# Optimization experiments

Measured on AMD Instinct MI355X. Metric: run time of the kernel, lower is better.

## Reference

```python
import jax, jax.numpy as jnp
import numpy as np

L, D, H, FF = 4, 256, 8, 4 * 256  # num_layers, d_model, nhead, ffn hidden
DK = D // H
EPS = 1e-5


def _ln(x, g, b):
    mu = jnp.mean(x, axis=-1, keepdims=True)
    var = jnp.mean(jnp.square(x - mu), axis=-1, keepdims=True)
    return (x - mu) * jax.lax.rsqrt(var + EPS) * g + b


def setup_inputs() -> dict:
    key = jax.random.key(0)
    ks = jax.random.split(key, 16)
    B, N = 8, 1024
    s = 0.02
    return {
        "x": jax.random.normal(ks[0], (B, N, D), jnp.float32),
        "coords": jax.random.normal(ks[1], (B, N, 3), jnp.float32),
        "Wq": jax.random.normal(ks[2], (L, D, D), jnp.float32) * s,
        "bq": jnp.zeros((L, D), jnp.float32),
        "Wk": jax.random.normal(ks[3], (L, D, D), jnp.float32) * s,
        "bk": jnp.zeros((L, D), jnp.float32),
        "Wv": jax.random.normal(ks[4], (L, D, D), jnp.float32) * s,
        "bv": jnp.zeros((L, D), jnp.float32),
        "alpha": jnp.full((L,), 0.1, jnp.float32),
        "W1": jax.random.normal(ks[5], (L, D, FF), jnp.float32) * s,
        "b1": jnp.zeros((L, FF), jnp.float32),
        "W2": jax.random.normal(ks[6], (L, FF, D), jnp.float32) * s,
        "b2": jnp.zeros((L, D), jnp.float32),
        "g1": jnp.ones((L, D), jnp.float32),
        "be1": jnp.zeros((L, D), jnp.float32),
        "g2": jnp.ones((L, D), jnp.float32),
        "be2": jnp.zeros((L, D), jnp.float32),
    }


def reference(x, coords, Wq, bq, Wk, bk, Wv, bv, alpha, W1, b1, W2, b2, g1, be1, g2, be2):
    B, N, _ = x.shape
    # Per-batch pairwise coord dot products (same math as the BN x BN matmul
    # sliced per batch in the original, computed without the cross-batch waste).
    G0 = jnp.einsum("bnc,bmc->bnm", coords, coords)  # [B,N,N]
    scale = 1.0 / jnp.sqrt(jnp.float32(DK))
    for i in range(L):
        q = (x @ Wq[i] + bq[i]).reshape(B, N, H, DK)
        k = (x @ Wk[i] + bk[i]).reshape(B, N, H, DK)
        v = (x @ Wv[i] + bv[i]).reshape(B, N, H, DK)
        scores = jnp.einsum("bnhd,bmhd->bhnm", q, k) * scale + (alpha[i] * G0)[:, None]
        attn = jax.nn.softmax(scores, axis=-1)
        out = jnp.einsum("bhnm,bmhd->bnhd", attn, v).reshape(B, N, D)
        x = _ln(x + out, g1[i], be1[i])
        ff = jnp.maximum(x @ W1[i] + b1[i], 0.0) @ W2[i] + b2[i]
        x = _ln(x + ff, g2[i], be2[i])
    return x
```

## Files before the change

### kernel.cpp

```cpp
#include <hip/hip_runtime.h>
#include <hip/hip_bf16.h>

#define BB 8
#define NN 1024
#define DD 256
#define HH 8
#define DK 32
#define FFN 1024
#define NLAYERS 4
#define MM (BB * NN)
#define ROW_ELEMS (MM * DD)

#define QSCALE 0.2550655192922103f
#define LOG2E  1.4426950408889634f

typedef unsigned short ushort_t;
typedef __attribute__((ext_vector_type(8))) short bf16x8;
typedef __attribute__((ext_vector_type(4))) short bf16x4;
typedef __attribute__((ext_vector_type(4))) float f32x4;

__device__ __forceinline__ f32x4 mfma16(bf16x4 a, bf16x4 b, f32x4 c) {
#if __has_builtin(__builtin_amdgcn_mfma_f32_16x16x16bf16_1k)
    return __builtin_amdgcn_mfma_f32_16x16x16bf16_1k(a, b, c, 0, 0, 0);
#elif defined(__AMDGCN__)
    f32x4 d;
    asm volatile("v_mfma_f32_16x16x16_bf16 %0, %1, %2, %3"
                 : "=v"(d)
                 : "v"(a), "v"(b), "v"(c));
    return d;
#else
    return c;
#endif
}

__device__ __forceinline__ ushort_t f2b(float f) {
    __hip_bfloat16 h = __float2bfloat16(f);
    return *reinterpret_cast<ushort_t*>(&h);
}

__device__ __forceinline__ float fast_exp2(float x) {
#if __has_builtin(__builtin_amdgcn_exp2f)
    return __builtin_amdgcn_exp2f(x);
#else
    return exp2f(x);
#endif
}

__device__ __forceinline__ void async_ld16(const void* g, void* l) {
    __builtin_amdgcn_global_load_lds((const __attribute__((address_space(1))) void*)g,
                                     (__attribute__((address_space(3))) void*)l, 16, 0, 0);
}

#define PREP_BLOCKS (NLAYERS * 707)
#define COPY_BLOCKS (ROW_ELEMS / 4 / 256)
__global__ __launch_bounds__(256) void setup_kernel(const float* __restrict__ Wq,
                                                    const float* __restrict__ Wk,
                                                    const float* __restrict__ Wv,
                                                    const float* __restrict__ W1,
                                                    const float* __restrict__ W2,
                                                    const float* __restrict__ bq,
                                                    const float* __restrict__ bk,
                                                    const float* __restrict__ bv,
                                                    ushort_t* __restrict__ wqkvt,
                                                    ushort_t* __restrict__ w1t,
                                                    ushort_t* __restrict__ w2t,
                                                    float* __restrict__ bqkv,
                                                    const float4* __restrict__ in,
                                                    float4* __restrict__ xf,
                                                    ushort4* __restrict__ xb,
                                                    const float* __restrict__ coords,
                                                    ushort_t* __restrict__ Qa,
                                                    ushort_t* __restrict__ Ka) {
    const int tid = threadIdx.x;
    __shared__ float tile[32][33];

    if (blockIdx.x < PREP_BLOCKS) {
        const int id = blockIdx.x;
        const int layer = id / 707;
        const int r = id % 707;

        if (r >= 704) {
            const int chunk = r - 704;
            const float* src = (chunk == 0) ? bq : (chunk == 1) ? bk : bv;
            bqkv[layer * 768 + chunk * 256 + tid] = src[layer * 256 + tid];
            return;
        }

        const float* src;
        ushort_t* dst;
        int R, C, x, y;
        if (r < 192) {
            const int w = r >> 6, rr = r & 63;
            src = ((w == 0) ? Wq : (w == 1) ? Wk : Wv) + (size_t)layer * 65536;
            dst = wqkvt + (size_t)layer * 196608 + w * 65536;
            R = 256; C = 256; x = rr & 7; y = rr >> 3;
        } else if (r < 448) {
            const int rr = r - 192;
            src = W1 + (size_t)layer * 262144;
            dst = w1t + (size_t)layer * 262144;
            R = 256; C = 1024; x = rr & 31; y = rr >> 5;
        } else {
            const int rr = r - 448;
            src = W2 + (size_t)layer * 262144;
            dst = w2t + (size_t)layer * 262144;
            R = 1024; C = 256; x = rr & 7; y = rr >> 3;
        }
        const int r0 = y * 32, c0 = x * 32;
        const int tx = tid & 31, ty = tid >> 5;
#pragma unroll
        for (int i = 0; i < 4; ++i)
            tile[ty + 8 * i][tx] = src[(size_t)(r0 + ty + 8 * i) * C + (c0 + tx)];
        __syncthreads();
#pragma unroll
        for (int i = 0; i < 4; ++i)
            dst[(size_t)(c0 + ty + 8 * i) * R + (r0 + tx)] = f2b(tile[tx][ty + 8 * i]);
    } else {
        const int cb = blockIdx.x - PREP_BLOCKS;
        const int i = cb * 256 + tid;
        {
            float4 v = in[i];
            xf[i] = v;
            ushort4 b = {f2b(v.x), f2b(v.y), f2b(v.z), f2b(v.w)};
            xb[i] = b;
        }
        if (cb < 256) {
            const int id = cb * 256 + tid;
            const int bh = id >> 10, n = id & 1023;
            const int b = bh >> 3;
            ushort_t buf[32];
#pragma unroll
            for (int d = 0; d < 32; ++d) buf[d] = 0;
            buf[0] = f2b(coords[(size_t)(b * NN + n) * 3 + 0]);
            buf[1] = f2b(coords[(size_t)(b * NN + n) * 3 + 1]);
            buf[2] = f2b(coords[(size_t)(b * NN + n) * 3 + 2]);
            ushort_t* kp = Ka + ((size_t)bh * NN + n) * 64 + 32;
            ushort_t* qp = Qa + ((size_t)bh * NN + n) * 64 + 32;
            const uint4* b4 = (const uint4*)buf;
            uint4 z4 = {0u, 0u, 0u, 0u};
#pragma unroll
            for (int c = 0; c < 4; ++c) {
                *(uint4*)(kp + c * 8) = b4[c];
                *(uint4*)(qp + c * 8) = z4;
            }
        }
    }
}

template <int MODE, int BM>
__global__ __launch_bounds__(256) void mfma_gemm_kernel(const ushort_t* __restrict__ A,
                                                        const ushort_t* __restrict__ Bt,
                                                        const float* __restrict__ bias,
                                                        void* __restrict__ C0,
                                                        void* __restrict__ C1,
                                                        void* __restrict__ C2,
                                                        const float* __restrict__ coords,
                                                        const float* __restrict__ alpha, int layer,
                                                        int K, int ldc) {
    constexpr int NI = BM / 32;
    __shared__ ushort_t As0[2][BM * 32];
    __shared__ ushort_t As1[2][BM * 32];
    __shared__ ushort_t Bs0[2][128 * 32];
    __shared__ ushort_t Bs1[2][128 * 32];

    const int t    = threadIdx.x;
    const int bm   = blockIdx.y * BM;
    const int bn   = blockIdx.x * 128;
    const int wave = t >> 6, lane = t & 63;
    const int wm   = (wave >> 1) * (BM / 2), wn = (wave & 1) * 64;
    const int quad = lane >> 4, l16 = lane & 15;

    const int srow = t >> 2;
    const int scol = (t & 3) * 8;

    f32x4 acc[NI][4];
#pragma unroll
    for (int i = 0; i < NI; ++i)
#pragma unroll
        for (int j = 0; j < 4; ++j) {
            f32x4 z = {0.f, 0.f, 0.f, 0.f};
            acc[i][j] = z;
        }

    auto stage = [&](int pb, int k0) {
        async_ld16(A + (size_t)(bm + srow) * K + k0 + scol, As0[pb] + wave * 512);
        if constexpr (BM == 128)
            async_ld16(A + (size_t)(bm + 64 + srow) * K + k0 + scol, As0[pb] + 2048 + wave * 512);
        async_ld16(Bt + (size_t)(bn + srow) * K + k0 + scol, Bs0[pb] + wave * 512);
        async_ld16(Bt + (size_t)(bn + 64 + srow) * K + k0 + scol, Bs0[pb] + 2048 + wave * 512);
        async_ld16(A + (size_t)(bm + srow) * K + k0 + 32 + scol, As1[pb] + wave * 512);
        if constexpr (BM == 128)
            async_ld16(A + (size_t)(bm + 64 + srow) * K + k0 + 32 + scol, As1[pb] + 2048 + wave * 512);
        async_ld16(Bt + (size_t)(bn + srow) * K + k0 + 32 + scol, Bs1[pb] + wave * 512);
        async_ld16(Bt + (size_t)(bn + 64 + srow) * K + k0 + 32 + scol, Bs1[pb] + 2048 + wave * 512);
    };

    stage(0, 0);
    int pb = 0;
    for (int k0 = 0; k0 < K; k0 += 64, pb ^= 1) {
        __syncthreads();

        if (k0 + 64 < K) stage(pb ^ 1, k0 + 64);

        bf16x8 af0[NI], af1[NI], bf0[4], bf1[4];
#pragma unroll
        for (int i = 0; i < NI; ++i) {
            af0[i] = *(const bf16x8*)(As0[pb] + (wm + i * 16 + l16) * 32 + quad * 8);
            af1[i] = *(const bf16x8*)(As1[pb] + (wm + i * 16 + l16) * 32 + quad * 8);
        }
#pragma unroll
        for (int j = 0; j < 4; ++j) {
            bf0[j] = *(const bf16x8*)(Bs0[pb] + (wn + j * 16 + l16) * 32 + quad * 8);
            bf1[j] = *(const bf16x8*)(Bs1[pb] + (wn + j * 16 + l16) * 32 + quad * 8);
        }
#pragma unroll
        for (int i = 0; i < NI; ++i)
#pragma unroll
            for (int j = 0; j < 4; ++j) {
                acc[i][j] = __builtin_amdgcn_mfma_f32_16x16x32_bf16(af0[i], bf0[j], acc[i][j], 0, 0, 0);
                acc[i][j] = __builtin_amdgcn_mfma_f32_16x16x32_bf16(af1[i], bf1[j], acc[i][j], 0, 0, 0);
            }
    }

    const float av = (MODE == 2) ? alpha[layer] : 0.f;

#pragma unroll
    for (int j = 0; j < 4; ++j) {
        const int col = bn + wn + j * 16 + l16;
        const float bsv = bias[col];
#pragma unroll
        for (int i = 0; i < NI; ++i) {
            const int row0 = bm + wm + i * 16 + quad * 4;
            if (MODE == 2) {
                const int bb2 = row0 >> 10, nn0 = row0 & 1023;
                const int which = col >> 8, rem = col & 255;
                const int h = rem >> 5, d = rem & 31;
                const size_t bh = (size_t)((bb2 << 3) + h);
                if (which == 2) {
                    ushort4 pk;
                    pk.x = f2b(acc[i][j][0] + bsv);
                    pk.y = f2b(acc[i][j][1] + bsv);
                    pk.z = f2b(acc[i][j][2] + bsv);
                    pk.w = f2b(acc[i][j][3] + bsv);
                    *(ushort4*)&((ushort_t*)C2)[(bh * DK + d) * NN + nn0] = pk;
                } else {
#pragma unroll
                    for (int r = 0; r < 4; ++r) {
                        const float v = acc[i][j][r] + bsv;
                        const int nn = nn0 + r;
                        if (which == 0) {
                            ((ushort_t*)C0)[(bh * NN + nn) * 64 + d] = f2b(v * QSCALE);
                            if (d < 3)
                                ((ushort_t*)C0)[(bh * NN + nn) * 64 + 32 + d] =
                                    f2b(av * LOG2E * coords[(size_t)(bb2 * NN + nn) * 3 + d]);
                        } else {
                            ((ushort_t*)C1)[(bh * NN + nn) * 64 + d] = f2b(v);
                        }
                    }
                }
            } else {
#pragma unroll
                for (int r = 0; r < 4; ++r) {
                    float v = acc[i][j][r] + bsv;
                    if (MODE == 0)
                        ((float*)C0)[(size_t)(row0 + r) * ldc + col] = v;
                    else
                        ((ushort_t*)C0)[(size_t)(row0 + r) * ldc + col] = f2b(fmaxf(v, 0.f));
                }
            }
        }
    }
}

template <int DO_QKV>
__global__ __launch_bounds__(512) void ffn_ln_kernel(const float* __restrict__ aout,
                                                     const float* __restrict__ xfin,
                                                     const ushort_t* __restrict__ W1t,
                                                     const ushort_t* __restrict__ W2t,
                                                     const float* __restrict__ g1,
                                                     const float* __restrict__ be1,
                                                     const float* __restrict__ b1,
                                                     const float* __restrict__ b2,
                                                     const float* __restrict__ g2,
                                                     const float* __restrict__ be2,
                                                     float* __restrict__ xout,
                                                     const ushort_t* __restrict__ Wqkvt,
                                                     const float* __restrict__ bqkv,
                                                     const float* __restrict__ coords,
                                                     const float* __restrict__ alpha, int qlayer,
                                                     ushort_t* __restrict__ Qa,
                                                     ushort_t* __restrict__ Ka,
                                                     ushort_t* __restrict__ Vt) {
    __shared__ ushort_t Ha[8][32][32];
    __shared__ ushort_t Asf[8][32][32];
    __shared__ ushort_t Bs0[2][256 * 32];
    __shared__ ushort_t Bs1[2][256 * 32];
    __shared__ float Ya[32][260];
    __shared__ float redS[8][32];
    __shared__ float redQ[8][32];

    const int t = threadIdx.x;
    const int bm = blockIdx.x * 32;
    const int wave = t >> 6, lane = t & 63;
    const int quad = lane >> 4, l16 = lane & 15;
    const int wn = wave * 32;
    const int scol = (t & 3) * 8;

    auto stageB1 = [&](int pb, int nc, int ks) {
        const int nbase = nc * 256;
        const int k0 = ks * 64;
#pragma unroll
        for (int c = 0; c < 2; ++c) {
            const int brow = nbase + c * 128 + (t >> 2);
            async_ld16(W1t + (size_t)brow * 256 + k0 + scol, Bs0[pb] + c * 4096 + wave * 512);
            async_ld16(W1t + (size_t)brow * 256 + k0 + 32 + scol, Bs1[pb] + c * 4096 + wave * 512);
        }
    };
    auto stageB2 = [&](int pb, int nc, int ks) {
        const int k0 = nc * 256 + ks * 64;
#pragma unroll
        for (int c = 0; c < 2; ++c) {
            const int brow = c * 128 + (t >> 2);
            async_ld16(W2t + (size_t)brow * 1024 + k0 + scol, Bs0[pb] + c * 4096 + wave * 512);
            async_ld16(W2t + (size_t)brow * 1024 + k0 + 32 + scol, Bs1[pb] + c * 4096 + wave * 512);
        }
    };
    auto stage = [&](int pb, int st) {
        const int group = st >> 2, ks = st & 3, nc = group >> 1;
        if (!(group & 1)) stageB1(pb, nc, ks);
        else stageB2(pb, nc, ks);
    };
    auto stageQKV = [&](int pb, int qst) {
        const int chunk = qst >> 2, ks = qst & 3;
#pragma unroll
        for (int c = 0; c < 2; ++c) {
            const int brow = chunk * 256 + c * 128 + (t >> 2);
            async_ld16(Wqkvt + (size_t)brow * 256 + ks * 64 + scol, Bs0[pb] + c * 4096 + wave * 512);
            async_ld16(Wqkvt + (size_t)brow * 256 + ks * 64 + 32 + scol, Bs1[pb] + c * 4096 + wave * 512);
        }
    };

    stage(0, 0);

#pragma unroll
    for (int rr = 0; rr < 4; ++rr) {
        const int row = wave * 4 + rr;
        const size_t base = (size_t)(bm + row) * DD + lane * 4;

        float4 xv = *(const float4*)(xfin + base);
        float4 dl = *(const float4*)(aout + base);
        float v0 = xv.x + dl.x, v1 = xv.y + dl.y, v2 = xv.z + dl.z, v3 = xv.w + dl.w;

        float s = v0 + v1 + v2 + v3;
#pragma unroll
        for (int off = 32; off; off >>= 1) s += __shfl_xor(s, off);
        const float mean = s * (1.0f / 256.0f);

        float d0 = v0 - mean, d1 = v1 - mean, d2 = v2 - mean, d3 = v3 - mean;
        float s2 = d0 * d0 + d1 * d1 + d2 * d2 + d3 * d3;
#pragma unroll
        for (int off = 32; off; off >>= 1) s2 += __shfl_xor(s2, off);
        const float rs = rsqrtf(s2 * (1.0f / 256.0f) + 1e-5f);

        float4 gv = *(const float4*)(g1 + lane * 4);
        float4 bv = *(const float4*)(be1 + lane * 4);
        float y0 = d0 * rs * gv.x + bv.x;
        float y1 = d1 * rs * gv.y + bv.y;
        float y2 = d2 * rs * gv.z + bv.z;
        float y3 = d3 * rs * gv.w + bv.w;

        float4 yv = {y0, y1, y2, y3};
        *(float4*)&Ya[row][lane * 4] = yv;
        const int col0 = lane * 4;
        ushort4 yb = {f2b(y0), f2b(y1), f2b(y2), f2b(y3)};
        *(ushort4*)&Asf[col0 >> 5][row][col0 & 31] = yb;
    }

    f32x4 acc1[2][2], acc2[2][2];
#pragma unroll
    for (int i = 0; i < 2; ++i)
#pragma unroll
        for (int j = 0; j < 2; ++j) {
            f32x4 z = {0.f, 0.f, 0.f, 0.f};
            acc1[i][j] = z;
            acc2[i][j] = z;
        }

    int pb = 0;
    for (int st = 0; st < 32; ++st, pb ^= 1) {
        __syncthreads();
        if (st < 31) stage(pb ^ 1, st + 1);
        else if (DO_QKV) stageQKV(pb ^ 1, 0);

        const int group = st >> 2, ks = st & 3;
        const bool ff1 = !(group & 1);

        bf16x8 af0[2], af1[2], bf0[2], bf1[2];
#pragma unroll
        for (int i = 0; i < 2; ++i) {
            if (ff1) {
                af0[i] = *(const bf16x8*)&Asf[2 * ks][i * 16 + l16][quad * 8];
                af1[i] = *(const bf16x8*)&Asf[2 * ks + 1][i * 16 + l16][quad * 8];
            } else {
                af0[i] = *(const bf16x8*)&Ha[2 * ks][i * 16 + l16][quad * 8];
                af1[i] = *(const bf16x8*)&Ha[2 * ks + 1][i * 16 + l16][quad * 8];
            }
        }
#pragma unroll
        for (int j = 0; j < 2; ++j) {
            bf0[j] = *(const bf16x8*)(Bs0[pb] + (wn + j * 16 + l16) * 32 + quad * 8);
            bf1[j] = *(const bf16x8*)(Bs1[pb] + (wn + j * 16 + l16) * 32 + quad * 8);
        }

        if (ff1) {
#pragma unroll
            for (int i = 0; i < 2; ++i)
#pragma unroll
                for (int j = 0; j < 2; ++j) {
                    acc1[i][j] = __builtin_amdgcn_mfma_f32_16x16x32_bf16(af0[i], bf0[j], acc1[i][j], 0, 0, 0);
                    acc1[i][j] = __builtin_amdgcn_mfma_f32_16x16x32_bf16(af1[i], bf1[j], acc1[i][j], 0, 0, 0);
                }
            if (ks == 3) {
                const int nc = group >> 1;
#pragma unroll
                for (int j = 0; j < 2; ++j) {
                    const int col = nc * 256 + wn + j * 16 + l16;
                    const float bj = b1[col];
#pragma unroll
                    for (int i = 0; i < 2; ++i)
#pragma unroll
                        for (int r = 0; r < 4; ++r) {
                            const int row = i * 16 + quad * 4 + r;
                            Ha[wave][row][j * 16 + l16] =
                                f2b(fmaxf(acc1[i][j][r] + bj, 0.f));
                        }
                }
#pragma unroll
                for (int i = 0; i < 2; ++i)
#pragma unroll
                    for (int j = 0; j < 2; ++j) {
                        f32x4 z = {0.f, 0.f, 0.f, 0.f};
                        acc1[i][j] = z;
                    }
            }
        } else {
#pragma unroll
            for (int i = 0; i < 2; ++i)
#pragma unroll
                for (int j = 0; j < 2; ++j) {
                    acc2[i][j] = __builtin_amdgcn_mfma_f32_16x16x32_bf16(af0[i], bf0[j], acc2[i][j], 0, 0, 0);
                    acc2[i][j] = __builtin_amdgcn_mfma_f32_16x16x32_bf16(af1[i], bf1[j], acc2[i][j], 0, 0, 0);
                }
        }
    }

    float mean[2][4], rstd[2][4];

    {
        float sum_[2][4];
#pragma unroll
        for (int i = 0; i < 2; ++i)
#pragma unroll
            for (int r = 0; r < 4; ++r) sum_[i][r] = 0.f;
#pragma unroll
        for (int j = 0; j < 2; ++j) {
            const int col = wn + j * 16 + l16;
            const float bj = b2[col];
#pragma unroll
            for (int i = 0; i < 2; ++i) {
#pragma unroll
                for (int r = 0; r < 4; ++r) {
                    const int row = i * 16 + quad * 4 + r;
                    const float v = acc2[i][j][r] + bj + Ya[row][col];
                    acc2[i][j][r] = v;
                    sum_[i][r] += v;
                }
            }
        }
#pragma unroll
        for (int i = 0; i < 2; ++i)
#pragma unroll
            for (int r = 0; r < 4; ++r) {
                float s = sum_[i][r];
                s += __shfl_xor(s, 1);
                s += __shfl_xor(s, 2);
                s += __shfl_xor(s, 4);
                s += __shfl_xor(s, 8);
                sum_[i][r] = s;
            }
        if (l16 == 0) {
#pragma unroll
            for (int i = 0; i < 2; ++i)
#pragma unroll
                for (int r = 0; r < 4; ++r) redS[wave][i * 16 + quad * 4 + r] = sum_[i][r];
        }
        __syncthreads();
#pragma unroll
        for (int i = 0; i < 2; ++i)
#pragma unroll
            for (int r = 0; r < 4; ++r) {
                const int rl = i * 16 + quad * 4 + r;
                float s = 0.f;
#pragma unroll
                for (int w = 0; w < 8; ++w) s += redS[w][rl];
                mean[i][r] = s * (1.0f / 256.0f);
            }
    }

    {
        float sq_[2][4];
#pragma unroll
        for (int i = 0; i < 2; ++i)
#pragma unroll
            for (int r = 0; r < 4; ++r) sq_[i][r] = 0.f;
#pragma unroll
        for (int j = 0; j < 2; ++j)
#pragma unroll
            for (int i = 0; i < 2; ++i)
#pragma unroll
                for (int r = 0; r < 4; ++r) {
                    const float d = acc2[i][j][r] - mean[i][r];
                    sq_[i][r] += d * d;
                }
#pragma unroll
        for (int i = 0; i < 2; ++i)
#pragma unroll
            for (int r = 0; r < 4; ++r) {
                float s = sq_[i][r];
                s += __shfl_xor(s, 1);
                s += __shfl_xor(s, 2);
                s += __shfl_xor(s, 4);
                s += __shfl_xor(s, 8);
                sq_[i][r] = s;
            }
        if (l16 == 0) {
#pragma unroll
            for (int i = 0; i < 2; ++i)
#pragma unroll
                for (int r = 0; r < 4; ++r) redQ[wave][i * 16 + quad * 4 + r] = sq_[i][r];
        }
        __syncthreads();
#pragma unroll
        for (int i = 0; i < 2; ++i)
#pragma unroll
            for (int r = 0; r < 4; ++r) {
                const int rl = i * 16 + quad * 4 + r;
                float s = 0.f;
#pragma unroll
                for (int w = 0; w < 8; ++w) s += redQ[w][rl];
                rstd[i][r] = rsqrtf(s * (1.0f / 256.0f) + 1e-5f);
            }
    }

#pragma unroll
    for (int j = 0; j < 2; ++j) {
        const int col = wn + j * 16 + l16;
        const float gv = g2[col];
        const float bev = be2[col];
#pragma unroll
        for (int i = 0; i < 2; ++i) {
            const int row = bm + i * 16 + quad * 4;
#pragma unroll
            for (int r = 0; r < 4; ++r) {
                const float y = (acc2[i][j][r] - mean[i][r]) * rstd[i][r] * gv + bev;
                xout[(size_t)(row + r) * DD + col] = y;
                if (DO_QKV)
                    Asf[wave][i * 16 + quad * 4 + r][j * 16 + l16] = f2b(y);
            }
        }
    }

    if constexpr (DO_QKV) {
        const float av = alpha[qlayer];
        f32x4 acc3[2][2];
#pragma unroll
        for (int i = 0; i < 2; ++i)
#pragma unroll
            for (int j = 0; j < 2; ++j) {
                f32x4 z = {0.f, 0.f, 0.f, 0.f};
                acc3[i][j] = z;
            }

        for (int qst = 0; qst < 12; ++qst, pb ^= 1) {
            __syncthreads();
            if (qst < 11) stageQKV(pb ^ 1, qst + 1);

            const int ks = qst & 3;
            bf16x8 af0[2], af1[2], bf0[2], bf1[2];
#pragma unroll
            for (int i = 0; i < 2; ++i) {
                af0[i] = *(const bf16x8*)&Asf[2 * ks][i * 16 + l16][quad * 8];
                af1[i] = *(const bf16x8*)&Asf[2 * ks + 1][i * 16 + l16][quad * 8];
            }
#pragma unroll
            for (int j = 0; j < 2; ++j) {
                bf0[j] = *(const bf16x8*)(Bs0[pb] + (wn + j * 16 + l16) * 32 + quad * 8);
                bf1[j] = *(const bf16x8*)(Bs1[pb] + (wn + j * 16 + l16) * 32 + quad * 8);
            }
#pragma unroll
            for (int i = 0; i < 2; ++i)
#pragma unroll
                for (int j = 0; j < 2; ++j) {
                    acc3[i][j] = __builtin_amdgcn_mfma_f32_16x16x32_bf16(af0[i], bf0[j], acc3[i][j], 0, 0, 0);
                    acc3[i][j] = __builtin_amdgcn_mfma_f32_16x16x32_bf16(af1[i], bf1[j], acc3[i][j], 0, 0, 0);
                }

            if (ks == 3) {
                const int which = qst >> 2;
#pragma unroll
                for (int j = 0; j < 2; ++j) {
                    const int rem = wn + j * 16 + l16;
                    const float bsv = bqkv[which * 256 + rem];
                    const int h = rem >> 5, d = rem & 31;
#pragma unroll
                    for (int i = 0; i < 2; ++i) {
                        const int row0 = bm + i * 16 + quad * 4;
                        const int bb2 = row0 >> 10, nn0 = row0 & 1023;
                        const size_t bh = (size_t)((bb2 << 3) + h);
                        if (which == 2) {
                            ushort4 pk;
                            pk.x = f2b(acc3[i][j][0] + bsv);
                            pk.y = f2b(acc3[i][j][1] + bsv);
                            pk.z = f2b(acc3[i][j][2] + bsv);
                            pk.w = f2b(acc3[i][j][3] + bsv);
                            *(ushort4*)&Vt[(bh * DK + d) * NN + nn0] = pk;
                        } else {
#pragma unroll
                            for (int r = 0; r < 4; ++r) {
                                const float v = acc3[i][j][r] + bsv;
                                const int nn = nn0 + r;
                                if (which == 0) {
                                    Qa[(bh * NN + nn) * 64 + d] = f2b(v * QSCALE);
                                    if (d < 3)
                                        Qa[(bh * NN + nn) * 64 + 32 + d] =
                                            f2b(av * LOG2E *
                                                coords[(size_t)(bb2 * NN + nn) * 3 + d]);
                                } else {
                                    Ka[(bh * NN + nn) * 64 + d] = f2b(v);
                                }
                            }
                        }
                    }
                }
#pragma unroll
                for (int i = 0; i < 2; ++i)
#pragma unroll
                    for (int j = 0; j < 2; ++j) {
                        f32x4 z = {0.f, 0.f, 0.f, 0.f};
                        acc3[i][j] = z;
                    }
            }
        }
    }
}

__global__ __launch_bounds__(256, 2) void attn8_kernel(const ushort_t* __restrict__ Qa,
                                                       const ushort_t* __restrict__ Ka,
                                                       const ushort_t* __restrict__ Vt,
                                                       float* __restrict__ aout) {
    const int b = blockIdx.x, h = blockIdx.y, n0 = blockIdx.z * 64;
    const int t = threadIdx.x, wave = t >> 6, lane = t & 63;
    const int quad = lane >> 4, l16 = lane & 15;
    const int bh = b * HH + h;

    __shared__ __align__(16) char smem[56320];
    ushort_t (*Ks)[64][72] = (ushort_t (*)[64][72])smem;
    ushort_t (*Vs)[32][72] = (ushort_t (*)[32][72])(smem + 36864);
    float    (*Om)[64][36] = (float (*)[64][36])smem;
    float    (*Lm)[64]     = (float (*)[64])(smem + 55296);

    bf16x8 aq[4][2];
#pragma unroll
    for (int s = 0; s < 4; ++s) {
        const ushort_t* qp = Qa + ((size_t)bh * NN + n0 + s * 16 + l16) * 64 + quad * 8;
        aq[s][0] = *(const bf16x8*)qp;
        aq[s][1] = *(const bf16x8*)(qp + 32);
    }

    const f32x4 z = {0.f, 0.f, 0.f, 0.f};
    f32x4 acc[4][2];
    float lsum[4];
#pragma unroll
    for (int s = 0; s < 4; ++s) { acc[s][0] = z; acc[s][1] = z; lsum[s] = 0.f; }

    const ushort_t* kg = Ka + ((size_t)bh * NN + wave * 256) * 64;
    const ushort_t* vg = Vt + (size_t)bh * DK * NN + wave * 256;

    const int srow = lane >> 3, sch = (lane & 7) * 8;

    uint4 kreg[8], vreg[4];
#pragma unroll
    for (int i = 0; i < 8; ++i) kreg[i] = *(const uint4*)(kg + (size_t)(i * 8 + srow) * 64 + sch);
#pragma unroll
    for (int i = 0; i < 4; ++i) vreg[i] = *(const uint4*)(vg + (size_t)(i * 8 + srow) * NN + sch);

    for (int kt = 0; kt < 4; ++kt) {
#pragma unroll
        for (int i = 0; i < 8; ++i) *(uint4*)&Ks[wave][i * 8 + srow][sch] = kreg[i];
#pragma unroll
        for (int i = 0; i < 4; ++i) *(uint4*)&Vs[wave][i * 8 + srow][sch] = vreg[i];

        bf16x8 bk0[4], bk1[4];
#pragma unroll
        for (int jt = 0; jt < 4; ++jt) {
            bk0[jt] = *(const bf16x8*)&Ks[wave][jt * 16 + l16][quad * 8];
            bk1[jt] = *(const bf16x8*)&Ks[wave][jt * 16 + l16][32 + quad * 8];
        }
        bf16x4 vfrag[2][4];
#pragma unroll
        for (int g = 0; g < 2; ++g)
#pragma unroll
            for (int jt = 0; jt < 4; ++jt)
                vfrag[g][jt] = *(const bf16x4*)&Vs[wave][g * 16 + l16][jt * 16 + quad * 4];

        if (kt < 3) {
            const ushort_t* kg2 = kg + (size_t)(kt + 1) * 64 * 64;
            const ushort_t* vg2 = vg + (kt + 1) * 64;
#pragma unroll
            for (int i = 0; i < 8; ++i)
                kreg[i] = *(const uint4*)(kg2 + (size_t)(i * 8 + srow) * 64 + sch);
#pragma unroll
            for (int i = 0; i < 4; ++i)
                vreg[i] = *(const uint4*)(vg2 + (size_t)(i * 8 + srow) * NN + sch);
        }

#pragma unroll
        for (int s = 0; s < 4; ++s) {
            f32x4 st[4];
            __builtin_amdgcn_s_setprio(1);
#pragma unroll
            for (int jt = 0; jt < 4; ++jt) {
                st[jt] = __builtin_amdgcn_mfma_f32_16x16x32_bf16(bk0[jt], aq[s][0], z, 0, 0, 0);
                st[jt] = __builtin_amdgcn_mfma_f32_16x16x32_bf16(bk1[jt], aq[s][1], st[jt], 0, 0, 0);
            }
            __builtin_amdgcn_s_setprio(0);
            bf16x4 pf[4];
            float ls = 0.f;
#pragma unroll
            for (int jt = 0; jt < 4; ++jt) {
                float e0 = fast_exp2(st[jt][0]);
                float e1 = fast_exp2(st[jt][1]);
                float e2 = fast_exp2(st[jt][2]);
                float e3 = fast_exp2(st[jt][3]);
                ls += (e0 + e1) + (e2 + e3);
                pf[jt][0] = (short)f2b(e0);
                pf[jt][1] = (short)f2b(e1);
                pf[jt][2] = (short)f2b(e2);
                pf[jt][3] = (short)f2b(e3);
            }
            lsum[s] += ls;
            __builtin_amdgcn_s_setprio(1);
#pragma unroll
            for (int jt = 0; jt < 4; ++jt) {
                acc[s][0] = mfma16(vfrag[0][jt], pf[jt], acc[s][0]);
                acc[s][1] = mfma16(vfrag[1][jt], pf[jt], acc[s][1]);
            }
            __builtin_amdgcn_s_setprio(0);
        }
    }

#pragma unroll
    for (int s = 0; s < 4; ++s) {
        lsum[s] += __shfl_xor(lsum[s], 16);
        lsum[s] += __shfl_xor(lsum[s], 32);
    }

    __syncthreads();
    if (quad == 0) {
#pragma unroll
        for (int s = 0; s < 4; ++s) Lm[wave][s * 16 + l16] = lsum[s];
    }

#pragma unroll
    for (int s = 0; s < 4; ++s) {
        const int q = s * 16 + l16;
#pragma unroll
        for (int g = 0; g < 2; ++g) {
            float4 v = {acc[s][g][0], acc[s][g][1], acc[s][g][2], acc[s][g][3]};
            *(float4*)&Om[wave][q][g * 16 + quad * 4] = v;
        }
    }
    __syncthreads();

    {
        const int q = t >> 2, dseg = (t & 3) * 8;
        const float inv = 1.0f / (Lm[0][q] + Lm[1][q] + Lm[2][q] + Lm[3][q]);
        float* op = aout + (size_t)(b * NN + n0 + q) * DD + h * DK + dseg;
        float4 s0 = {0.f, 0.f, 0.f, 0.f}, s1 = {0.f, 0.f, 0.f, 0.f};
#pragma unroll
        for (int w = 0; w < 4; ++w) {
            float4 a = *(const float4*)&Om[w][q][dseg];
            float4 c = *(const float4*)&Om[w][q][dseg + 4];
            s0.x += a.x; s0.y += a.y; s0.z += a.z; s0.w += a.w;
            s1.x += c.x; s1.y += c.y; s1.z += c.z; s1.w += c.w;
        }
        float4 o0 = {s0.x * inv, s0.y * inv, s0.z * inv, s0.w * inv};
        float4 o1 = {s1.x * inv, s1.y * inv, s1.z * inv, s1.w * inv};
        *(float4*)op = o0;
        *(float4*)(op + 4) = o1;
    }
}

extern "C" void kernel_launch(void* const* d_in, const int* in_sizes, int n_in,
                              void* d_out, int out_size, void* d_ws, size_t ws_size,
                              hipStream_t stream) {
    const float* x      = (const float*)d_in[0];
    const float* coords = (const float*)d_in[1];
    const float* Wq     = (const float*)d_in[2];
    const float* bq     = (const float*)d_in[3];
    const float* Wk     = (const float*)d_in[4];
    const float* bk     = (const float*)d_in[5];
    const float* Wv     = (const float*)d_in[6];
    const float* bv     = (const float*)d_in[7];
    const float* alpha  = (const float*)d_in[8];
    const float* W1     = (const float*)d_in[9];
    const float* b1     = (const float*)d_in[10];
    const float* W2     = (const float*)d_in[11];
    const float* b2     = (const float*)d_in[12];
    const float* g1     = (const float*)d_in[13];
    const float* be1    = (const float*)d_in[14];
    const float* g2     = (const float*)d_in[15];
    const float* be2    = (const float*)d_in[16];

    float* ws = (float*)d_ws;
    float*    xf    = ws;
    ushort_t* xb    = (ushort_t*)(ws + 2097152);
    ushort_t* Qa    = (ushort_t*)(ws + 3145728);
    ushort_t* Ka    = (ushort_t*)(ws + 5242880);
    ushort_t* Vt    = (ushort_t*)(ws + 7340032);
    float*    aout  = ws + 8388608;
    ushort_t* wqkvt = (ushort_t*)(ws + 10485760);
    ushort_t* w1t   = (ushort_t*)(ws + 10878976);
    ushort_t* w2t   = (ushort_t*)(ws + 11403264);
    float*    bqkv  = ws + 11927552;

    setup_kernel<<<PREP_BLOCKS + COPY_BLOCKS, 256, 0, stream>>>(
        Wq, Wk, Wv, W1, W2, bq, bk, bv, wqkvt, w1t, w2t, bqkv,
        (const float4*)x, (float4*)xf, (ushort4*)xb, coords, Qa, Ka);

    mfma_gemm_kernel<2, 64><<<dim3(6, 128), 256, 0, stream>>>(
        xb, wqkvt, bqkv, Qa, Ka, Vt, coords, alpha, 0, 256, 0);

    for (int i = 0; i < NLAYERS; ++i) {
        attn8_kernel<<<dim3(8, 8, 16), 256, 0, stream>>>(Qa, Ka, Vt, aout);

        if (i < NLAYERS - 1) {
            ffn_ln_kernel<1><<<MM / 32, 512, 0, stream>>>(
                aout, xf, w1t + (size_t)i * 262144, w2t + (size_t)i * 262144,
                g1 + i * 256, be1 + i * 256, b1 + i * 1024, b2 + i * 256,
                g2 + i * 256, be2 + i * 256, xf,
                wqkvt + (size_t)(i + 1) * 196608, bqkv + (i + 1) * 768,
                coords, alpha, i + 1, Qa, Ka, Vt);
        } else {
            ffn_ln_kernel<0><<<MM / 32, 512, 0, stream>>>(
                aout, xf, w1t + (size_t)i * 262144, w2t + (size_t)i * 262144,
                g1 + i * 256, be1 + i * 256, b1 + i * 1024, b2 + i * 256,
                g2 + i * 256, be2 + i * 256, (float*)d_out,
                nullptr, nullptr, nullptr, nullptr, 0, nullptr, nullptr, nullptr);
        }
    }
}
```

Baseline: 359.7 us.

## Halve FFN row tile to 16 and single-buffer weight staging for occupancy

```diff
diff --git a/kernel.cpp b/kernel.cpp
--- a/kernel.cpp
+++ b/kernel.cpp
@@ -272,78 +272,78 @@
 }
 
 template <int DO_QKV>
-__global__ __launch_bounds__(512) void ffn_ln_kernel(const float* __restrict__ aout,
-                                                     const float* __restrict__ xfin,
-                                                     const ushort_t* __restrict__ W1t,
-                                                     const ushort_t* __restrict__ W2t,
-                                                     const float* __restrict__ g1,
-                                                     const float* __restrict__ be1,
-                                                     const float* __restrict__ b1,
-                                                     const float* __restrict__ b2,
-                                                     const float* __restrict__ g2,
-                                                     const float* __restrict__ be2,
-                                                     float* __restrict__ xout,
-                                                     const ushort_t* __restrict__ Wqkvt,
-                                                     const float* __restrict__ bqkv,
-                                                     const float* __restrict__ coords,
-                                                     const float* __restrict__ alpha, int qlayer,
-                                                     ushort_t* __restrict__ Qa,
-                                                     ushort_t* __restrict__ Ka,
-                                                     ushort_t* __restrict__ Vt) {
-    __shared__ ushort_t Ha[8][32][32];
-    __shared__ ushort_t Asf[8][32][32];
-    __shared__ ushort_t Bs0[2][256 * 32];
-    __shared__ ushort_t Bs1[2][256 * 32];
-    __shared__ float Ya[32][260];
-    __shared__ float redS[8][32];
-    __shared__ float redQ[8][32];
+__global__ __launch_bounds__(512, 4) void ffn_ln_kernel(const float* __restrict__ aout,
+                                                        const float* __restrict__ xfin,
+                                                        const ushort_t* __restrict__ W1t,
+                                                        const ushort_t* __restrict__ W2t,
+                                                        const float* __restrict__ g1,
+                                                        const float* __restrict__ be1,
+                                                        const float* __restrict__ b1,
+                                                        const float* __restrict__ b2,
+                                                        const float* __restrict__ g2,
+                                                        const float* __restrict__ be2,
+                                                        float* __restrict__ xout,
+                                                        const ushort_t* __restrict__ Wqkvt,
+                                                        const float* __restrict__ bqkv,
+                                                        const float* __restrict__ coords,
+                                                        const float* __restrict__ alpha, int qlayer,
+                                                        ushort_t* __restrict__ Qa,
+                                                        ushort_t* __restrict__ Ka,
+                                                        ushort_t* __restrict__ Vt) {
+    __shared__ ushort_t Ha[8][16][32];
+    __shared__ ushort_t Asf[8][16][32];
+    __shared__ ushort_t Bs0[256 * 32];
+    __shared__ ushort_t Bs1[256 * 32];
+    __shared__ float Ya[16][260];
+    __shared__ float redS[8][16];
+    __shared__ float redQ[8][16];
 
     const int t = threadIdx.x;
-    const int bm = blockIdx.x * 32;
+    const int bm = blockIdx.x * 16;
     const int wave = t >> 6, lane = t & 63;
     const int quad = lane >> 4, l16 = lane & 15;
     const int wn = wave * 32;
     const int scol = (t & 3) * 8;
 
-    auto stageB1 = [&](int pb, int nc, int ks) {
+    auto stageB1 = [&](int nc, int ks) {
         const int nbase = nc * 256;
         const int k0 = ks * 64;
 #pragma unroll
         for (int c = 0; c < 2; ++c) {
             const int brow = nbase + c * 128 + (t >> 2);
-            async_ld16(W1t + (size_t)brow * 256 + k0 + scol, Bs0[pb] + c * 4096 + wave * 512);
-            async_ld16(W1t + (size_t)brow * 256 + k0 + 32 + scol, Bs1[pb] + c * 4096 + wave * 512);
+            async_ld16(W1t + (size_t)brow * 256 + k0 + scol, Bs0 + c * 4096 + wave * 512);
+            async_ld16(W1t + (size_t)brow * 256 + k0 + 32 + scol, Bs1 + c * 4096 + wave * 512);
         }
     };
-    auto stageB2 = [&](int pb, int nc, int ks) {
+    auto stageB2 = [&](int nc, int ks) {
         const int k0 = nc * 256 + ks * 64;
 #pragma unroll
         for (int c = 0; c < 2; ++c) {
             const int brow = c * 128 + (t >> 2);
-            async_ld16(W2t + (size_t)brow * 1024 + k0 + scol, Bs0[pb] + c * 4096 + wave * 512);
-            async_ld16(W2t + (size_t)brow * 1024 + k0 + 32 + scol, Bs1[pb] + c * 4096 + wave * 512);
+            async_ld16(W2t + (size_t)brow * 1024 + k0 + scol, Bs0 + c * 4096 + wave * 512);
+            async_ld16(W2t + (size_t)brow * 1024 + k0 + 32 + scol, Bs1 + c * 4096 + wave * 512);
         }
     };
-    auto stage = [&](int pb, int st) {
+    auto stageFFN = [&](int st) {
         const int group = st >> 2, ks = st & 3, nc = group >> 1;
-        if (!(group & 1)) stageB1(pb, nc, ks);
-        else stageB2(pb, nc, ks);
+        if (!(group & 1)) stageB1(nc, ks);
+        else stageB2(nc, ks);
     };
-    auto stageQKV = [&](int pb, int qst) {
+    auto stageQKV = [&](int qst) {
         const int chunk = qst >> 2, ks = qst & 3;
 #pragma unroll
         for (int c = 0; c < 2; ++c) {
             const int brow = chunk * 256 + c * 128 + (t >> 2);
-            async_ld16(Wqkvt + (size_t)brow * 256 + ks * 64 + scol, Bs0[pb] + c * 4096 + wave * 512);
-            async_ld16(Wqkvt + (size_t)brow * 256 + ks * 64 + 32 + scol, Bs1[pb] + c * 4096 + wave * 512);
+            async_ld16(Wqkvt + (size_t)brow * 256 + ks * 64 + scol, Bs0 + c * 4096 + wave * 512);
+            async_ld16(Wqkvt + (size_t)brow * 256 + ks * 64 + 32 + scol, Bs1 + c * 4096 + wave * 512);
         }
     };
 
-    stage(0, 0);
-
-#pragma unroll
-    for (int rr = 0; rr < 4; ++rr) {
-        const int row = wave * 4 + rr;
+    stageFFN(0);
+
+#pragma unroll
+    for (int rr = 0; rr < 2; ++rr) {
+        const int row = wave * 2 + rr;
         const size_t base = (size_t)(bm + row) * DD + lane * 4;
 
         float4 xv = *(const float4*)(xfin + base);
@@ -375,50 +375,40 @@
         *(ushort4*)&Asf[col0 >> 5][row][col0 & 31] = yb;
     }
 
-    f32x4 acc1[2][2], acc2[2][2];
-#pragma unroll
-    for (int i = 0; i < 2; ++i)
-#pragma unroll
-        for (int j = 0; j < 2; ++j) {
-            f32x4 z = {0.f, 0.f, 0.f, 0.f};
-            acc1[i][j] = z;
-            acc2[i][j] = z;
-        }
-
-    int pb = 0;
-    for (int st = 0; st < 32; ++st, pb ^= 1) {
+    f32x4 acc1[2], acc2[2];
+#pragma unroll
+    for (int j = 0; j < 2; ++j) {
+        f32x4 z = {0.f, 0.f, 0.f, 0.f};
+        acc1[j] = z;
+        acc2[j] = z;
+    }
+
+    for (int st = 0; st < 32; ++st) {
         __syncthreads();
-        if (st < 31) stage(pb ^ 1, st + 1);
-        else if (DO_QKV) stageQKV(pb ^ 1, 0);
 
         const int group = st >> 2, ks = st & 3;
         const bool ff1 = !(group & 1);
 
-        bf16x8 af0[2], af1[2], bf0[2], bf1[2];
-#pragma unroll
-        for (int i = 0; i < 2; ++i) {
-            if (ff1) {
-                af0[i] = *(const bf16x8*)&Asf[2 * ks][i * 16 + l16][quad * 8];
-                af1[i] = *(const bf16x8*)&Asf[2 * ks + 1][i * 16 + l16][quad * 8];
-            } else {
-                af0[i] = *(const bf16x8*)&Ha[2 * ks][i * 16 + l16][quad * 8];
-                af1[i] = *(const bf16x8*)&Ha[2 * ks + 1][i * 16 + l16][quad * 8];
-            }
+        bf16x8 af0, af1, bf0[2], bf1[2];
+        if (ff1) {
+            af0 = *(const bf16x8*)&Asf[2 * ks][l16][quad * 8];
+            af1 = *(const bf16x8*)&Asf[2 * ks + 1][l16][quad * 8];
+        } else {
+            af0 = *(const bf16x8*)&Ha[2 * ks][l16][quad * 8];
+            af1 = *(const bf16x8*)&Ha[2 * ks + 1][l16][quad * 8];
         }
 #pragma unroll
         for (int j = 0; j < 2; ++j) {
-            bf0[j] = *(const bf16x8*)(Bs0[pb] + (wn + j * 16 + l16) * 32 + quad * 8);
-            bf1[j] = *(const bf16x8*)(Bs1[pb] + (wn + j * 16 + l16) * 32 + quad * 8);
+            bf0[j] = *(const bf16x8*)(Bs0 + (wn + j * 16 + l16) * 32 + quad * 8);
+            bf1[j] = *(const bf16x8*)(Bs1 + (wn + j * 16 + l16) * 32 + quad * 8);
         }
 
         if (ff1) {
 #pragma unroll
-            for (int i = 0; i < 2; ++i)
-#pragma unroll
-                for (int j = 0; j < 2; ++j) {
-                    acc1[i][j] = __builtin_amdgcn_mfma_f32_16x16x32_bf16(af0[i], bf0[j], acc1[i][j], 0, 0, 0);
-                    acc1[i][j] = __builtin_amdgcn_mfma_f32_16x16x32_bf16(af1[i], bf1[j], acc1[i][j], 0, 0, 0);
-                }
+            for (int j = 0; j < 2; ++j) {
+                acc1[j] = __builtin_amdgcn_mfma_f32_16x16x32_bf16(af0, bf0[j], acc1[j], 0, 0, 0);
+                acc1[j] = __builtin_amdgcn_mfma_f32_16x16x32_bf16(af1, bf1[j], acc1[j], 0, 0, 0);
+            }
             if (ks == 3) {
                 const int nc = group >> 1;
 #pragma unroll
@@ -426,129 +416,105 @@
                     const int col = nc * 256 + wn + j * 16 + l16;
                     const float bj = b1[col];
 #pragma unroll
-                    for (int i = 0; i < 2; ++i)
-#pragma unroll
-                        for (int r = 0; r < 4; ++r) {
-                            const int row = i * 16 + quad * 4 + r;
-                            Ha[wave][row][j * 16 + l16] =
-                                f2b(fmaxf(acc1[i][j][r] + bj, 0.f));
-                        }
+                    for (int r = 0; r < 4; ++r) {
+                        const int row = quad * 4 + r;
+                        Ha[wave][row][j * 16 + l16] = f2b(fmaxf(acc1[j][r] + bj, 0.f));
+                    }
                 }
 #pragma unroll
-                for (int i = 0; i < 2; ++i)
-#pragma unroll
-                    for (int j = 0; j < 2; ++j) {
-                        f32x4 z = {0.f, 0.f, 0.f, 0.f};
-                        acc1[i][j] = z;
-                    }
+                for (int j = 0; j < 2; ++j) {
+                    f32x4 z = {0.f, 0.f, 0.f, 0.f};
+                    acc1[j] = z;
+                }
             }
         } else {
 #pragma unroll
-            for (int i = 0; i < 2; ++i)
-#pragma unroll
-                for (int j = 0; j < 2; ++j) {
-                    acc2[i][j] = __builtin_amdgcn_mfma_f32_16x16x32_bf16(af0[i], bf0[j], acc2[i][j], 0, 0, 0);
-                    acc2[i][j] = __builtin_amdgcn_mfma_f32_16x16x32_bf16(af1[i], bf1[j], acc2[i][j], 0, 0, 0);
-                }
-        }
-    }
-
-    float mean[2][4], rstd[2][4];
+            for (int j = 0; j < 2; ++j) {
+                acc2[j] = __builtin_amdgcn_mfma_f32_16x16x32_bf16(af0, bf0[j], acc2[j], 0, 0, 0);
+                acc2[j] = __builtin_amdgcn_mfma_f32_16x16x32_bf16(af1, bf1[j], acc2[j], 0, 0, 0);
+            }
+        }
+
+        __syncthreads();
+        if (st + 1 < 32) stageFFN(st + 1);
+        else if (DO_QKV) stageQKV(0);
+    }
+
+    float mean[4], rstd[4];
 
     {
-        float sum_[2][4];
-#pragma unroll
-        for (int i = 0; i < 2; ++i)
-#pragma unroll
-            for (int r = 0; r < 4; ++r) sum_[i][r] = 0.f;
+        float sum_[4];
+#pragma unroll
+        for (int r = 0; r < 4; ++r) sum_[r] = 0.f;
 #pragma unroll
         for (int j = 0; j < 2; ++j) {
             const int col = wn + j * 16 + l16;
             const float bj = b2[col];
 #pragma unroll
-            for (int i = 0; i < 2; ++i) {
-#pragma unroll
-                for (int r = 0; r < 4; ++r) {
-                    const int row = i * 16 + quad * 4 + r;
-                    const float v = acc2[i][j][r] + bj + Ya[row][col];
-                    acc2[i][j][r] = v;
-                    sum_[i][r] += v;
-                }
-            }
-        }
-#pragma unroll
-        for (int i = 0; i < 2; ++i)
-#pragma unroll
             for (int r = 0; r < 4; ++r) {
-                float s = sum_[i][r];
-                s += __shfl_xor(s, 1);
-                s += __shfl_xor(s, 2);
-                s += __shfl_xor(s, 4);
-                s += __shfl_xor(s, 8);
-                sum_[i][r] = s;
-            }
+                const int row = quad * 4 + r;
+                const float v = acc2[j][r] + bj + Ya[row][col];
+                acc2[j][r] = v;
+                sum_[r] += v;
+            }
+        }
+#pragma unroll
+        for (int r = 0; r < 4; ++r) {
+            float s = sum_[r];
+            s += __shfl_xor(s, 1);
+            s += __shfl_xor(s, 2);
+            s += __shfl_xor(s, 4);
+            s += __shfl_xor(s, 8);
+            sum_[r] = s;
+        }
         if (l16 == 0) {
 #pragma unroll
-            for (int i = 0; i < 2; ++i)
-#pragma unroll
-                for (int r = 0; r < 4; ++r) redS[wave][i * 16 + quad * 4 + r] = sum_[i][r];
+            for (int r = 0; r < 4; ++r) redS[wave][quad * 4 + r] = sum_[r];
         }
         __syncthreads();
 #pragma unroll
-        for (int i = 0; i < 2; ++i)
+        for (int r = 0; r < 4; ++r) {
+            const int rl = quad * 4 + r;
+            float s = 0.f;
+#pragma unroll
+            for (int w = 0; w < 8; ++w) s += redS[w][rl];
+            mean[r] = s * (1.0f / 256.0f);
+        }
+    }
+
+    {
+        float sq_[4];
+#pragma unroll
+        for (int r = 0; r < 4; ++r) sq_[r] = 0.f;
+#pragma unroll
+        for (int j = 0; j < 2; ++j)
 #pragma unroll
             for (int r = 0; r < 4; ++r) {
-                const int rl = i * 16 + quad * 4 + r;
-                float s = 0.f;
-#pragma unroll
-                for (int w = 0; w < 8; ++w) s += redS[w][rl];
-                mean[i][r] = s * (1.0f / 256.0f);
-            }
-    }
-
-    {
-        float sq_[2][4];
-#pragma unroll
-        for (int i = 0; i < 2; ++i)
-#pragma unroll
-            for (int r = 0; r < 4; ++r) sq_[i][r] = 0.f;
-#pragma unroll
-        for (int j = 0; j < 2; ++j)
-#pragma unroll
-            for (int i = 0; i < 2; ++i)
-#pragma unroll
-                for (int r = 0; r < 4; ++r) {
-                    const float d = acc2[i][j][r] - mean[i][r];
-                    sq_[i][r] += d * d;
-                }
-#pragma unroll
-        for (int i = 0; i < 2; ++i)
-#pragma unroll
-            for (int r = 0; r < 4; ++r) {
-                float s = sq_[i][r];
-                s += __shfl_xor(s, 1);
-                s += __shfl_xor(s, 2);
-                s += __shfl_xor(s, 4);
-                s += __shfl_xor(s, 8);
-                sq_[i][r] = s;
-            }
+                const float d = acc2[j][r] - mean[r];
+                sq_[r] += d * d;
+            }
+#pragma unroll
+        for (int r = 0; r < 4; ++r) {
+            float s = sq_[r];
+            s += __shfl_xor(s, 1);
+            s += __shfl_xor(s, 2);
+            s += __shfl_xor(s, 4);
+            s += __shfl_xor(s, 8);
+            sq_[r] = s;
+        }
         if (l16 == 0) {
 #pragma unroll
-            for (int i = 0; i < 2; ++i)
-#pragma unroll
-                for (int r = 0; r < 4; ++r) redQ[wave][i * 16 + quad * 4 + r] = sq_[i][r];
+            for (int r = 0; r < 4; ++r) redQ[wave][quad * 4 + r] = sq_[r];
         }
         __syncthreads();
 #pragma unroll
-        for (int i = 0; i < 2; ++i)
-#pragma unroll
-            for (int r = 0; r < 4; ++r) {
-                const int rl = i * 16 + quad * 4 + r;
-                float s = 0.f;
-#pragma unroll
-                for (int w = 0; w < 8; ++w) s += redQ[w][rl];
-                rstd[i][r] = rsqrtf(s * (1.0f / 256.0f) + 1e-5f);
-            }
+        for (int r = 0; r < 4; ++r) {
+            const int rl = quad * 4 + r;
+            float s = 0.f;
+#pragma unroll
+            for (int w = 0; w < 8; ++w) s += redQ[w][rl];
+            rstd[r] = rsqrtf(s * (1.0f / 256.0f) + 1e-5f);
+        }
     }
 
 #pragma unroll
@@ -557,52 +523,46 @@
         const float gv = g2[col];
         const float bev = be2[col];
 #pragma unroll
-        for (int i = 0; i < 2; ++i) {
-            const int row = bm + i * 16 + quad * 4;
-#pragma unroll
-            for (int r = 0; r < 4; ++r) {
-                const float y = (acc2[i][j][r] - mean[i][r]) * rstd[i][r] * gv + bev;
-                xout[(size_t)(row + r) * DD + col] = y;
-                if (DO_QKV)
-                    Asf[wave][i * 16 + quad * 4 + r][j * 16 + l16] = f2b(y);
-            }
+        for (int r = 0; r < 4; ++r) {
+            const int row = bm + quad * 4 + r;
+            const float y = (acc2[j][r] - mean[r]) * rstd[r] * gv + bev;
+            xout[(size_t)row * DD + col] = y;
+            if (DO_QKV)
+                Asf[wn >> 5][quad * 4 + r][j * 16 + l16] = f2b(y);
         }
     }
 
     if constexpr (DO_QKV) {
         const float av = alpha[qlayer];
-        f32x4 acc3[2][2];
-#pragma unroll
-        for (int i = 0; i < 2; ++i)
+        f32x4 acc3[2];
+#pragma unroll
+        for (int j = 0; j < 2; ++j) {
+            f32x4 z = {0.f, 0.f, 0.f, 0.f};
+            acc3[j] = z;
+        }
+
+        for (int qst = 0; qst < 12; ++qst) {
+            __syncthreads();
+
+            const int ks = qst & 3;
+            bf16x8 af0, af1, bf0[2], bf1[2];
+            af0 = *(const bf16x8*)&Asf[2 * ks][l16][quad * 8];
+            af1 = *(const bf16x8*)&Asf[2 * ks + 1][l16][quad * 8];
 #pragma unroll
             for (int j = 0; j < 2; ++j) {
-                f32x4 z = {0.f, 0.f, 0.f, 0.f};
-                acc3[i][j] = z;
-            }
-
-        for (int qst = 0; qst < 12; ++qst, pb ^= 1) {
-            __syncthreads();
-            if (qst < 11) stageQKV(pb ^ 1, qst + 1);
-
-            const int ks = qst & 3;
-            bf16x8 af0[2], af1[2], bf0[2], bf1[2];
-#pragma unroll
-            for (int i = 0; i < 2; ++i) {
-                af0[i] = *(const bf16x8*)&Asf[2 * ks][i * 16 + l16][quad * 8];
-                af1[i] = *(const bf16x8*)&Asf[2 * ks + 1][i * 16 + l16][quad * 8];
+                bf0[j] = *(const bf16x8*)(Bs0 + (wn + j * 16 + l16) * 32 + quad * 8);
+                bf1[j] = *(const bf16x8*)(Bs1 + (wn + j * 16 + l16) * 32 + quad * 8);
             }
 #pragma unroll
             for (int j = 0; j < 2; ++j) {
-                bf0[j] = *(const bf16x8*)(Bs0[pb] + (wn + j * 16 + l16) * 32 + quad * 8);
-                bf1[j] = *(const bf16x8*)(Bs1[pb] + (wn + j * 16 + l16) * 32 + quad * 8);
-            }
-#pragma unroll
-            for (int i = 0; i < 2; ++i)
-#pragma unroll
-                for (int j = 0; j < 2; ++j) {
-                    acc3[i][j] = __builtin_amdgcn_mfma_f32_16x16x32_bf16(af0[i], bf0[j], acc3[i][j], 0, 0, 0);
-                    acc3[i][j] = __builtin_amdgcn_mfma_f32_16x16x32_bf16(af1[i], bf1[j], acc3[i][j], 0, 0, 0);
-                }
+                acc3[j] = __builtin_amdgcn_mfma_f32_16x16x32_bf16(af0, bf0[j], acc3[j], 0, 0, 0);
+                acc3[j] = __builtin_amdgcn_mfma_f32_16x16x32_bf16(af1, bf1[j], acc3[j], 0, 0, 0);
+            }
+
+            if (qst + 1 < 12) {
+                __syncthreads();
+                stageQKV(qst + 1);
+            }
 
             if (ks == 3) {
                 const int which = qst >> 2;
@@ -611,43 +571,38 @@
                     const int rem = wn + j * 16 + l16;
                     const float bsv = bqkv[which * 256 + rem];
                     const int h = rem >> 5, d = rem & 31;
-#pragma unroll
-                    for (int i = 0; i < 2; ++i) {
-                        const int row0 = bm + i * 16 + quad * 4;
-                        const int bb2 = row0 >> 10, nn0 = row0 & 1023;
-                        const size_t bh = (size_t)((bb2 << 3) + h);
-                        if (which == 2) {
-                            ushort4 pk;
-                            pk.x = f2b(acc3[i][j][0] + bsv);
-                            pk.y = f2b(acc3[i][j][1] + bsv);
-                            pk.z = f2b(acc3[i][j][2] + bsv);
-                            pk.w = f2b(acc3[i][j][3] + bsv);
-                            *(ushort4*)&Vt[(bh * DK + d) * NN + nn0] = pk;
-                        } else {
-#pragma unroll
-                            for (int r = 0; r < 4; ++r) {
-                                const float v = acc3[i][j][r] + bsv;
-                                const int nn = nn0 + r;
-                                if (which == 0) {
-                                    Qa[(bh * NN + nn) * 64 + d] = f2b(v * QSCALE);
-                                    if (d < 3)
-                                        Qa[(bh * NN + nn) * 64 + 32 + d] =
-                                            f2b(av * LOG2E *
-                                                coords[(size_t)(bb2 * NN + nn) * 3 + d]);
-                                } else {
-                                    Ka[(bh * NN + nn) * 64 + d] = f2b(v);
-                                }
+                    const int row0 = bm + quad * 4;
+                    const int bb2 = row0 >> 10, nn0 = row0 & 1023;
+                    const size_t bh = (size_t)((bb2 << 3) + h);
+                    if (which == 2) {
+                        ushort4 pk;
+                        pk.x = f2b(acc3[j][0] + bsv);
+                        pk.y = f2b(acc3[j][1] + bsv);
+                        pk.z = f2b(acc3[j][2] + bsv);
+                        pk.w = f2b(acc3[j][3] + bsv);
+                        *(ushort4*)&Vt[(bh * DK + d) * NN + nn0] = pk;
+                    } else {
+#pragma unroll
+                        for (int r = 0; r < 4; ++r) {
+                            const float v = acc3[j][r] + bsv;
+                            const int nn = nn0 + r;
+                            if (which == 0) {
+                                Qa[(bh * NN + nn) * 64 + d] = f2b(v * QSCALE);
+                                if (d < 3)
+                                    Qa[(bh * NN + nn) * 64 + 32 + d] =
+                                        f2b(av * LOG2E *
+                                            coords[(size_t)(bb2 * NN + nn) * 3 + d]);
+                            } else {
+                                Ka[(bh * NN + nn) * 64 + d] = f2b(v);
                             }
                         }
                     }
                 }
 #pragma unroll
-                for (int i = 0; i < 2; ++i)
-#pragma unroll
-                    for (int j = 0; j < 2; ++j) {
-                        f32x4 z = {0.f, 0.f, 0.f, 0.f};
-                        acc3[i][j] = z;
-                    }
+                for (int j = 0; j < 2; ++j) {
+                    f32x4 z = {0.f, 0.f, 0.f, 0.f};
+                    acc3[j] = z;
+                }
             }
         }
     }
@@ -844,14 +799,14 @@
         attn8_kernel<<<dim3(8, 8, 16), 256, 0, stream>>>(Qa, Ka, Vt, aout);
 
         if (i < NLAYERS - 1) {
-            ffn_ln_kernel<1><<<MM / 32, 512, 0, stream>>>(
+            ffn_ln_kernel<1><<<MM / 16, 512, 0, stream>>>(
                 aout, xf, w1t + (size_t)i * 262144, w2t + (size_t)i * 262144,
                 g1 + i * 256, be1 + i * 256, b1 + i * 1024, b2 + i * 256,
                 g2 + i * 256, be2 + i * 256, xf,
                 wqkvt + (size_t)(i + 1) * 196608, bqkv + (i + 1) * 768,
                 coords, alpha, i + 1, Qa, Ka, Vt);
         } else {
-            ffn_ln_kernel<0><<<MM / 32, 512, 0, stream>>>(
+            ffn_ln_kernel<0><<<MM / 16, 512, 0, stream>>>(
                 aout, xf, w1t + (size_t)i * 262144, w2t + (size_t)i * 262144,
                 g1 + i * 256, be1 + i * 256, b1 + i * 1024, b2 + i * 256,
                 g2 + i * 256, be2 + i * 256, (float*)d_out,
```

Measured after the change: 385.8 us. +7.2%, slower.
